# Kernel tuning notes

Hardware: AMD Instinct MI355X
Metric: run time of the kernel (lower is better)

Reference implementation:

```python
import jax, jax.numpy as jnp
import numpy as np

# Dims: B batch, T snippets, DV visual feat (1024), DA audio feat (128),
# H hid_dim (128), DF ffn dim (512), KC classifier kernel (7)
B, T, DV, DA, H, DF, KC = 128, 256, 1024, 128, 128, 512, 7


def _xavier(key, shape, fan_in, fan_out):
    a = (6.0 / (fan_in + fan_out)) ** 0.5
    return jax.random.uniform(key, shape, jnp.float32, -a, a)


def setup_inputs() -> dict:
    key = jax.random.key(0)
    ks = jax.random.split(key, 9)
    return {
        "x": jax.random.normal(ks[0], (B, T, DV + DA), jnp.float32),
        # CrossAttention: q from audio (DA->H), k,v from visual (DV->H), out proj H->DV
        "Wq": _xavier(ks[1], (DA, H), DA, H), "bq": jnp.zeros((H,), jnp.float32),
        "Wk": _xavier(ks[2], (DV, H), DV, H), "bk": jnp.zeros((H,), jnp.float32),
        "Wv": _xavier(ks[3], (DV, H), DV, H), "bv": jnp.zeros((H,), jnp.float32),
        "Wo": _xavier(ks[4], (H, DV), H, DV), "bo": jnp.zeros((DV,), jnp.float32),
        # LayerNorm over modal_a=1024
        "ln_g": jnp.ones((DV,), jnp.float32), "ln_b": jnp.zeros((DV,), jnp.float32),
        # FFN: Conv1d(1024,512,1) -> GELU -> Conv1d(512,128,1) == two linears over channels
        "W1": _xavier(ks[5], (DV, DF), DV, DF), "b1": jnp.zeros((DF,), jnp.float32),
        "W2": _xavier(ks[6], (DF, H), DF, H), "b2": jnp.zeros((H,), jnp.float32),
        # Classifier: Conv1d(128, 1, kernel=7), OIH layout
        "Wc": _xavier(ks[7], (1, H, KC), H * KC, KC), "bc": jnp.zeros((1,), jnp.float32),
    }


def _distance_adj(t: int) -> jnp.ndarray:
    # adj[i, j] = exp(-|i - j| / e)  (DistanceAdj from the repo)
    idx = jnp.arange(t, dtype=jnp.float32)
    return jnp.exp(-jnp.abs(idx[:, None] - idx[None, :]) / jnp.float32(np.e))


def reference(x, Wq, bq, Wk, bk, Wv, bv, Wo, bo, ln_g, ln_b, W1, b1, W2, b2, Wc, bc):
    f_v = x[:, :, :DV]   # [B, T, 1024]
    f_a = x[:, :, DV:]   # [B, T, 128]
    adj = _distance_adj(T)  # [T, T], broadcast over batch

    # Cross attention: query from audio, key/value from visual, adjacency bias
    q = f_a @ Wq + bq                               # [B, T, H]
    k = f_v @ Wk + bk                               # [B, T, H]
    v = f_v @ Wv + bv                               # [B, T, H]
    scores = jnp.einsum('bqh,bkh->bqk', q, k) / jnp.sqrt(jnp.float32(H)) + adj
    attn = jax.nn.softmax(scores, axis=-1)
    ctx = jnp.einsum('bqk,bkh->bqh', attn, v)       # [B, T, H]
    ca_out = ctx @ Wo + bo                          # [B, T, 1024]

    # residual + LayerNorm(modal_a)
    h = f_v + ca_out
    mu = jnp.mean(h, axis=-1, keepdims=True)
    var = jnp.mean(jnp.square(h - mu), axis=-1, keepdims=True)
    h = (h - mu) * jax.lax.rsqrt(var + 1e-5) * ln_g + ln_b

    # conv1d(k=1) FFN: 1024 -> 512 -> GELU -> 128 (dropout = identity at eval)
    h = jax.nn.gelu(h @ W1 + b1, approximate=False) @ W2 + b2   # [B, T, 128]

    # causal left pad 6, then Conv1d(128 -> 1, kernel 7)
    hc = jnp.pad(jnp.transpose(h, (0, 2, 1)), ((0, 0), (0, 0), (KC - 1, 0)))  # [B, 128, T+6]
    logits = jax.lax.conv_general_dilated(
        hc, Wc, window_strides=(1,), padding='VALID',
        dimension_numbers=('NCH', 'OIH', 'NCH')) + bc[None, :, None]           # [B, 1, T]
    return jax.nn.sigmoid(logits[:, 0, :])                                      # [B, T]
```

## Files before the change

kernel.cpp:

```cpp
#include <hip/hip_runtime.h>
#include <hip/hip_bf16.h>
#include <math.h>

#define BB 128
#define TT 256
#define DV 1024
#define DA 128
#define HH 128
#define DF 512
#define KC 7
#define MM (BB*TT)

typedef __attribute__((ext_vector_type(8))) short    short8v;
typedef __attribute__((ext_vector_type(8))) _Float16 half8v;
typedef __attribute__((ext_vector_type(4))) float    float4v;

__device__ __forceinline__ float gelu_exact(float v) {
    return 0.5f * v * (1.0f + erff(v * 0.70710678118654752f));
}
__device__ __forceinline__ ushort f2h(float f) {
    _Float16 h = (_Float16)f;
    return __builtin_bit_cast(ushort, h);
}
__device__ __forceinline__ float h2f(ushort u) {
    _Float16 h = __builtin_bit_cast(_Float16, u);
    return (float)h;
}

__global__ __launch_bounds__(256) void wconv_kernel(const float* __restrict__ W,
                                                    ushort* __restrict__ Th,
                                                    int K, int N)
{
    __shared__ float sT[64][65];
    const int n0 = blockIdx.x * 64, k0 = blockIdx.y * 64;
    const int t = threadIdx.x;
    const int kk = t >> 4, n4 = (t & 15) * 4;
#pragma unroll
    for (int i = 0; i < 4; ++i) {
        float4 f = *(const float4*)(W + (size_t)(k0 + kk + i * 16) * N + n0 + n4);
        sT[kk + i * 16][n4 + 0] = f.x;
        sT[kk + i * 16][n4 + 1] = f.y;
        sT[kk + i * 16][n4 + 2] = f.z;
        sT[kk + i * 16][n4 + 3] = f.w;
    }
    __syncthreads();
    const int n = t >> 2, kq = (t & 3) * 16;
    ushort hh[16];
#pragma unroll
    for (int j = 0; j < 16; ++j) hh[j] = f2h(sT[kq + j][n]);
    ushort* dh = Th + (size_t)(n0 + n) * K + k0 + kq;
#pragma unroll
    for (int j = 0; j < 16; j += 4)
        *(ushort4*)(dh + j) = make_ushort4(hh[j], hh[j+1], hh[j+2], hh[j+3]);
}

template<int BM, int A_F32, int OUT>
__global__ __launch_bounds__(256) void mgemm(const void* __restrict__ Av, int lda,
                                             const ushort* __restrict__ Bt,
                                             const float* __restrict__ bias,
                                             void* __restrict__ Cv,
                                             int N, int K)
{
    constexpr int MF = BM / 32;
    __shared__ ushort Ah[4][BM][8];
    __shared__ ushort Bh[4][128][8];

    const int tid = threadIdx.x;
    const int l = tid & 63;
    const int w = tid >> 6;
    const int wrow = (w >> 1) * (MF * 16), wcol = (w & 1) * 64;
    const int m0 = blockIdx.y * BM, n0 = blockIdx.x * 128;

    float4v acc[MF][4];
#pragma unroll
    for (int m = 0; m < MF; ++m)
#pragma unroll
        for (int n = 0; n < 4; ++n) acc[m][n] = (float4v){0.f, 0.f, 0.f, 0.f};

    for (int k0 = 0; k0 < K; k0 += 32) {
        __syncthreads();
        if (A_F32) {
            if (BM == 128) {
                const int srow = tid >> 1, kh = (tid & 1) * 16;
                const float* Ap = (const float*)Av + (size_t)(m0 + srow) * lda + k0 + kh;
#pragma unroll
                for (int i = 0; i < 4; ++i) {
                    float4 f = *(const float4*)(Ap + i * 4);
                    *(ushort4*)&Ah[(kh >> 3) + (i >> 1)][srow][(i & 1) * 4] =
                        make_ushort4(f2h(f.x), f2h(f.y), f2h(f.z), f2h(f.w));
                }
            } else {
                const int srow = tid >> 2, ko = (tid & 3) * 8;
                const float* Ap = (const float*)Av + (size_t)(m0 + srow) * lda + k0 + ko;
#pragma unroll
                for (int i = 0; i < 2; ++i) {
                    float4 f = *(const float4*)(Ap + i * 4);
                    *(ushort4*)&Ah[ko >> 3][srow][i * 4] =
                        make_ushort4(f2h(f.x), f2h(f.y), f2h(f.z), f2h(f.w));
                }
            }
        } else {
            if (BM == 128) {
                const int srow = tid >> 1, kh = (tid & 1) * 16;
                const ushort* Ap = (const ushort*)Av + (size_t)(m0 + srow) * lda + k0 + kh;
                *(short8v*)&Ah[(kh >> 3) + 0][srow][0] = *(const short8v*)(Ap + 0);
                *(short8v*)&Ah[(kh >> 3) + 1][srow][0] = *(const short8v*)(Ap + 8);
            } else {
                const int srow = tid >> 2, ko = (tid & 3) * 8;
                const ushort* Ap = (const ushort*)Av + (size_t)(m0 + srow) * lda + k0 + ko;
                *(short8v*)&Ah[ko >> 3][srow][0] = *(const short8v*)Ap;
            }
        }
        {
            const int srow = tid >> 1, kh = (tid & 1) * 16;
            const ushort* Bp = Bt + (size_t)(n0 + srow) * K + k0 + kh;
            *(short8v*)&Bh[(kh >> 3) + 0][srow][0] = *(const short8v*)(Bp + 0);
            *(short8v*)&Bh[(kh >> 3) + 1][srow][0] = *(const short8v*)(Bp + 8);
        }
        __syncthreads();

        const int g = l >> 4, lr = l & 15;
        half8v af[MF], bf_[4];
#pragma unroll
        for (int m = 0; m < MF; ++m)
            af[m] = *(const half8v*)&Ah[g][wrow + m * 16 + lr][0];
#pragma unroll
        for (int n = 0; n < 4; ++n)
            bf_[n] = *(const half8v*)&Bh[g][wcol + n * 16 + lr][0];
#pragma unroll
        for (int m = 0; m < MF; ++m)
#pragma unroll
            for (int n = 0; n < 4; ++n)
                acc[m][n] = __builtin_amdgcn_mfma_f32_16x16x32_f16(af[m], bf_[n], acc[m][n], 0, 0, 0);
    }

    const int g = l >> 4, lr = l & 15;
#pragma unroll
    for (int n = 0; n < 4; ++n) {
        const int col = n0 + wcol + n * 16 + lr;
        const float bv = bias[col];
#pragma unroll
        for (int m = 0; m < MF; ++m) {
#pragma unroll
            for (int r = 0; r < 4; ++r) {
                const int row = m0 + wrow + m * 16 + g * 4 + r;
                float o = acc[m][n][r] + bv;
                if (OUT == 0)      ((float*)Cv)[(size_t)row * N + col] = o;
                else if (OUT == 1) ((ushort*)Cv)[(size_t)row * N + col] = f2h(gelu_exact(o));
                else               ((ushort*)Cv)[(size_t)row * N + col] = f2h(o);
            }
        }
    }
}

__global__ __launch_bounds__(256) void scores_kernel(const float* __restrict__ q,
                                                     const float* __restrict__ k,
                                                     float* __restrict__ S)
{
    const int kh = blockIdx.x;
    const int qh = blockIdx.y;
    const int b  = blockIdx.z;
    const int tid = threadIdx.x;
    const int tr = tid >> 4;
    const int tc = tid & 15;

    __shared__ float sA[32][68];
    __shared__ float sB[32][132];

    const float* Ab = q + ((size_t)b * TT + qh * 64) * HH;
    const float* Bb = k + ((size_t)b * TT + kh * 128) * HH;

    float acc[4][8];
#pragma unroll
    for (int i = 0; i < 4; ++i)
#pragma unroll
        for (int j = 0; j < 8; ++j) acc[i][j] = 0.0f;

    for (int k0 = 0; k0 < 128; k0 += 32) {
        __syncthreads();
#pragma unroll
        for (int ll = 0; ll < 2; ++ll) {
            int f = tid + ll * 256;
            int row = f >> 3, c4 = f & 7;
            float4 val = *(const float4*)(Ab + (size_t)row * HH + k0 + c4 * 4);
            sA[c4 * 4 + 0][row] = val.x;
            sA[c4 * 4 + 1][row] = val.y;
            sA[c4 * 4 + 2][row] = val.z;
            sA[c4 * 4 + 3][row] = val.w;
        }
#pragma unroll
        for (int ll = 0; ll < 4; ++ll) {
            int f = tid + ll * 256;
            int row = f >> 3, c4 = f & 7;
            float4 val = *(const float4*)(Bb + (size_t)row * HH + k0 + c4 * 4);
            sB[c4 * 4 + 0][row] = val.x;
            sB[c4 * 4 + 1][row] = val.y;
            sB[c4 * 4 + 2][row] = val.z;
            sB[c4 * 4 + 3][row] = val.w;
        }
        __syncthreads();
#pragma unroll
        for (int kk = 0; kk < 32; ++kk) {
            float4 a4 = *(const float4*)&sA[kk][tr * 4];
            float4 b0 = *(const float4*)&sB[kk][tc * 8];
            float4 b1 = *(const float4*)&sB[kk][tc * 8 + 4];
            float a[4]  = {a4.x, a4.y, a4.z, a4.w};
            float bb[8] = {b0.x, b0.y, b0.z, b0.w, b1.x, b1.y, b1.z, b1.w};
#pragma unroll
            for (int i = 0; i < 4; ++i)
#pragma unroll
                for (int j = 0; j < 8; ++j) acc[i][j] += a[i] * bb[j];
        }
    }

    const float scale = 0.088388347648318447f;
    const float inv_e = 0.36787944117144233f;
#pragma unroll
    for (int i = 0; i < 4; ++i) {
        int rq = qh * 64 + tr * 4 + i;
        float* srow = S + ((size_t)b * TT + rq) * TT + kh * 128 + tc * 8;
        float o[8];
#pragma unroll
        for (int j = 0; j < 8; ++j) {
            int ck = kh * 128 + tc * 8 + j;
            float adj = expf(-fabsf((float)(rq - ck)) * inv_e);
            o[j] = acc[i][j] * scale + adj;
        }
        *(float4*)srow       = make_float4(o[0], o[1], o[2], o[3]);
        *(float4*)(srow + 4) = make_float4(o[4], o[5], o[6], o[7]);
    }
}

__global__ __launch_bounds__(256) void softmax_kernel(float* __restrict__ S)
{
    const int row  = blockIdx.x * 4 + (threadIdx.x >> 6);
    const int lane = threadIdx.x & 63;
    float* p = S + (size_t)row * TT + lane * 4;
    float4 v = *(float4*)p;
    float m = fmaxf(fmaxf(v.x, v.y), fmaxf(v.z, v.w));
#pragma unroll
    for (int mask = 1; mask < 64; mask <<= 1) m = fmaxf(m, __shfl_xor(m, mask));
    float e0 = expf(v.x - m), e1 = expf(v.y - m), e2 = expf(v.z - m), e3 = expf(v.w - m);
    float s = e0 + e1 + e2 + e3;
#pragma unroll
    for (int mask = 1; mask < 64; mask <<= 1) s += __shfl_xor(s, mask);
    float inv = 1.0f / s;
    *(float4*)p = make_float4(e0 * inv, e1 * inv, e2 * inv, e3 * inv);
}

__global__ __launch_bounds__(256) void pv_kernel(const float* __restrict__ S,
                                                 const float* __restrict__ v,
                                                 ushort* __restrict__ ctx)
{
    const int qh = blockIdx.x;
    const int b  = blockIdx.y;
    const int tid = threadIdx.x;
    const int tr = tid >> 4;
    const int tc = tid & 15;

    __shared__ float sA[32][68];
    __shared__ float sB[32][132];

    const float* Ab = S + ((size_t)b * TT + qh * 64) * TT;
    const float* Bb = v + (size_t)b * TT * HH;

    float acc[4][8];
#pragma unroll
    for (int i = 0; i < 4; ++i)
#pragma unroll
        for (int j = 0; j < 8; ++j) acc[i][j] = 0.0f;

    for (int k0 = 0; k0 < 256; k0 += 32) {
        __syncthreads();
#pragma unroll
        for (int ll = 0; ll < 2; ++ll) {
            int f = tid + ll * 256;
            int row = f >> 3, c4 = f & 7;
            float4 val = *(const float4*)(Ab + (size_t)row * TT + k0 + c4 * 4);
            sA[c4 * 4 + 0][row] = val.x;
            sA[c4 * 4 + 1][row] = val.y;
            sA[c4 * 4 + 2][row] = val.z;
            sA[c4 * 4 + 3][row] = val.w;
        }
#pragma unroll
        for (int ll = 0; ll < 4; ++ll) {
            int f = tid + ll * 256;
            int row = f >> 5, c4 = f & 31;
            float4 val = *(const float4*)(Bb + (size_t)(k0 + row) * HH + c4 * 4);
            *(float4*)&sB[row][c4 * 4] = val;
        }
        __syncthreads();
#pragma unroll
        for (int kk = 0; kk < 32; ++kk) {
            float4 a4 = *(const float4*)&sA[kk][tr * 4];
            float4 b0 = *(const float4*)&sB[kk][tc * 8];
            float4 b1 = *(const float4*)&sB[kk][tc * 8 + 4];
            float a[4]  = {a4.x, a4.y, a4.z, a4.w};
            float bb[8] = {b0.x, b0.y, b0.z, b0.w, b1.x, b1.y, b1.z, b1.w};
#pragma unroll
            for (int i = 0; i < 4; ++i)
#pragma unroll
                for (int j = 0; j < 8; ++j) acc[i][j] += a[i] * bb[j];
        }
    }

#pragma unroll
    for (int i = 0; i < 4; ++i) {
        ushort* crow = ctx + ((size_t)b * TT + qh * 64 + tr * 4 + i) * HH + tc * 8;
        *(ushort4*)crow       = make_ushort4(f2h(acc[i][0]), f2h(acc[i][1]),
                                             f2h(acc[i][2]), f2h(acc[i][3]));
        *(ushort4*)(crow + 4) = make_ushort4(f2h(acc[i][4]), f2h(acc[i][5]),
                                             f2h(acc[i][6]), f2h(acc[i][7]));
    }
}

__global__ __launch_bounds__(256) void resln_kernel(const float* __restrict__ x,
                                                    const ushort* __restrict__ ca16,
                                                    ushort* __restrict__ h16,
                                                    const float* __restrict__ gam,
                                                    const float* __restrict__ bet)
{
    const int row = blockIdx.x;
    const int tid = threadIdx.x;
    const float4 f = *(const float4*)(x + (size_t)row * 1152 + tid * 4);
    const ushort4 c4v = *(const ushort4*)(ca16 + (size_t)row * 1024 + tid * 4);
    float4 h;
    h.x = f.x + h2f(c4v.x); h.y = f.y + h2f(c4v.y);
    h.z = f.z + h2f(c4v.z); h.w = f.w + h2f(c4v.w);

    float s  = h.x + h.y + h.z + h.w;
    float ss = h.x * h.x + h.y * h.y + h.z * h.z + h.w * h.w;
#pragma unroll
    for (int m = 1; m < 64; m <<= 1) {
        s  += __shfl_xor(s, m);
        ss += __shfl_xor(ss, m);
    }
    __shared__ float red[8];
    if ((tid & 63) == 0) {
        red[tid >> 6]       = s;
        red[4 + (tid >> 6)] = ss;
    }
    __syncthreads();
    s  = red[0] + red[1] + red[2] + red[3];
    ss = red[4] + red[5] + red[6] + red[7];
    const float mean = s * (1.0f / 1024.0f);
    const float var  = ss * (1.0f / 1024.0f) - mean * mean;
    const float rstd = 1.0f / sqrtf(var + 1e-5f);

    const float4 g4 = *(const float4*)(gam + tid * 4);
    const float4 b4 = *(const float4*)(bet + tid * 4);
    ushort* hout = h16 + (size_t)row * 1024 + tid * 4;
    *(ushort4*)hout = make_ushort4(
        f2h((h.x - mean) * rstd * g4.x + b4.x),
        f2h((h.y - mean) * rstd * g4.y + b4.y),
        f2h((h.z - mean) * rstd * g4.z + b4.z),
        f2h((h.w - mean) * rstd * g4.w + b4.w));
}

__global__ __launch_bounds__(256) void conv_kernel(const float* __restrict__ h2,
                                                   const float* __restrict__ Wc,
                                                   const float* __restrict__ bcp,
                                                   float* __restrict__ out)
{
    const int t0 = blockIdx.x * 64;
    const int b  = blockIdx.y;
    const int tid = threadIdx.x;

    __shared__ float sw[896];
    __shared__ float sh[70][130];
    __shared__ float red[4][64];

    for (int i = tid; i < 896; i += 256) sw[i] = Wc[i];
    for (int f = tid; f < 70 * 32; f += 256) {
        int rr = f >> 5, c4 = f & 31;
        int trow = t0 - 6 + rr;
        float4 val = make_float4(0.f, 0.f, 0.f, 0.f);
        if (trow >= 0)
            val = *(const float4*)(h2 + ((size_t)b * TT + trow) * HH + c4 * 4);
        sh[rr][c4 * 4 + 0] = val.x;
        sh[rr][c4 * 4 + 1] = val.y;
        sh[rr][c4 * 4 + 2] = val.z;
        sh[rr][c4 * 4 + 3] = val.w;
    }
    __syncthreads();

    const int tt  = tid & 63;
    const int grp = tid >> 6;
    const int i0  = grp * 32;
    float acc = 0.0f;
    for (int j = 0; j < 7; ++j) {
        const int srow2 = tt + j;
#pragma unroll
        for (int i2 = 0; i2 < 16; ++i2) {
            float2 hv = *(const float2*)&sh[srow2][i0 + i2 * 2];
            acc += hv.x * sw[(i0 + i2 * 2) * 7 + j] + hv.y * sw[(i0 + i2 * 2 + 1) * 7 + j];
        }
    }
    red[grp][tt] = acc;
    __syncthreads();
    if (grp == 0) {
        float tot = red[0][tt] + red[1][tt] + red[2][tt] + red[3][tt] + bcp[0];
        out[(size_t)b * TT + t0 + tt] = 1.0f / (1.0f + expf(-tot));
    }
}

extern "C" void kernel_launch(void* const* d_in, const int* in_sizes, int n_in,
                              void* d_out, int out_size, void* d_ws, size_t ws_size,
                              hipStream_t stream)
{
    const float* x   = (const float*)d_in[0];
    const float* Wq  = (const float*)d_in[1];
    const float* bq  = (const float*)d_in[2];
    const float* Wk  = (const float*)d_in[3];
    const float* bk  = (const float*)d_in[4];
    const float* Wv  = (const float*)d_in[5];
    const float* bv  = (const float*)d_in[6];
    const float* Wo  = (const float*)d_in[7];
    const float* bo  = (const float*)d_in[8];
    const float* lng = (const float*)d_in[9];
    const float* lnb = (const float*)d_in[10];
    const float* W1  = (const float*)d_in[11];
    const float* b1  = (const float*)d_in[12];
    const float* W2  = (const float*)d_in[13];
    const float* b2  = (const float*)d_in[14];
    const float* Wc  = (const float*)d_in[15];
    const float* bc  = (const float*)d_in[16];
    float* out = (float*)d_out;
    char* wsb = (char*)d_ws;

    ushort* WT   = (ushort*)wsb;
    const size_t oWq = 0,      oWk = 16384,  oWv = 147456;
    const size_t oWo = 278528, oW1 = 409600, oW2 = 933888;
    float*  qb   = (float*)(wsb + 4194304);
    float*  kb   = qb + 4194304;
    float*  vb   = kb + 4194304;
    ushort* ctxb = (ushort*)(wsb + 54525952);
    float*  Sbuf = (float*)(wsb + 62914560);
    ushort* ca16 = (ushort*)(wsb + 62914560);
    ushort* h16  = (ushort*)(wsb + 130023424);
    ushort* hf   = (ushort*)(wsb + 4194304);
    float*  h2   = (float*)(wsb + 37748736);

    dim3 thr(256);
    wconv_kernel<<<dim3(2, 2),  thr, 0, stream>>>(Wq, WT + oWq, 128, 128);
    wconv_kernel<<<dim3(2, 16), thr, 0, stream>>>(Wk, WT + oWk, 1024, 128);
    wconv_kernel<<<dim3(2, 16), thr, 0, stream>>>(Wv, WT + oWv, 1024, 128);
    wconv_kernel<<<dim3(16, 2), thr, 0, stream>>>(Wo, WT + oWo, 128, 1024);
    wconv_kernel<<<dim3(8, 16), thr, 0, stream>>>(W1, WT + oW1, 1024, 512);
    wconv_kernel<<<dim3(2, 8),  thr, 0, stream>>>(W2, WT + oW2, 512, 128);

    mgemm<64, 1, 0><<<dim3(1, 512), thr, 0, stream>>>(x,        1152, WT + oWk, bk, kb, 128, 1024);
    mgemm<64, 1, 0><<<dim3(1, 512), thr, 0, stream>>>(x,        1152, WT + oWv, bv, vb, 128, 1024);
    mgemm<64, 1, 0><<<dim3(1, 512), thr, 0, stream>>>(x + 1024, 1152, WT + oWq, bq, qb, 128, 128);
    scores_kernel <<<dim3(2, 4, 128), thr, 0, stream>>>(qb, kb, Sbuf);
    softmax_kernel<<<dim3(MM / 4),    thr, 0, stream>>>(Sbuf);
    pv_kernel     <<<dim3(4, 128),    thr, 0, stream>>>(Sbuf, vb, ctxb);
    mgemm<128, 0, 2><<<dim3(8, 256), thr, 0, stream>>>(ctxb, 128, WT + oWo, bo, ca16, 1024, 128);
    resln_kernel<<<dim3(MM), thr, 0, stream>>>(x, ca16, h16, lng, lnb);
    mgemm<128, 0, 1><<<dim3(4, 256), thr, 0, stream>>>(h16, 1024, WT + oW1, b1, hf, 512, 1024);
    mgemm<64, 0, 0><<<dim3(1, 512), thr, 0, stream>>>(hf, 512, WT + oW2, b2, h2, 128, 512);
    conv_kernel<<<dim3(4, 128), thr, 0, stream>>>(h2, Wc, bc, out);
}
```

Before: 568.8 us.

## Fuse K/V projections into one GEMM, stage epilogue via LDS, swizzle blocks

Concatenates the transposed Wk and Wv weights and their biases so one GEMM with N=256 produces an interleaved KV buffer, reading the visual activations once instead of twice. The scores and PV kernels now read K and V from that buffer with a 256 stride. The mgemm epilogue stages output tiles in shared memory and writes them back as vectorized rows instead of scattered scalar stores. It also remaps block indices so that neighbouring blocks are spread across XCDs. These add extra syncs and a tiny concat kernel.

```diff
diff --git a/kernel.cpp b/kernel.cpp
--- a/kernel.cpp
+++ b/kernel.cpp
@@ -54,6 +54,14 @@
         *(ushort4*)(dh + j) = make_ushort4(hh[j], hh[j+1], hh[j+2], hh[j+3]);
 }
 
+__global__ __launch_bounds__(256) void bcat_kernel(const float* __restrict__ a,
+                                                   const float* __restrict__ b,
+                                                   float* __restrict__ dst)
+{
+    const int t = threadIdx.x;
+    dst[t] = (t < 128) ? a[t] : b[t - 128];
+}
+
 template<int BM, int A_F32, int OUT>
 __global__ __launch_bounds__(256) void mgemm(const void* __restrict__ Av, int lda,
                                              const ushort* __restrict__ Bt,
@@ -62,14 +70,20 @@
                                              int N, int K)
 {
     constexpr int MF = BM / 32;
-    __shared__ ushort Ah[4][BM][8];
-    __shared__ ushort Bh[4][128][8];
+    __shared__ __align__(16) ushort smem[8192];
+    auto Ah = (ushort (*)[BM][8])(smem);
+    auto Bh = (ushort (*)[128][8])(smem + 4 * BM * 8);
+
+    const int nwg = gridDim.x * gridDim.y;
+    const int hid = blockIdx.y * gridDim.x + blockIdx.x;
+    const int d   = (hid & 7) * (nwg >> 3) + (hid >> 3);
+    const int bx  = d % gridDim.x, by = d / gridDim.x;
 
     const int tid = threadIdx.x;
     const int l = tid & 63;
     const int w = tid >> 6;
     const int wrow = (w >> 1) * (MF * 16), wcol = (w & 1) * 64;
-    const int m0 = blockIdx.y * BM, n0 = blockIdx.x * 128;
+    const int m0 = by * BM, n0 = bx * 128;
 
     float4v acc[MF][4];
 #pragma unroll
@@ -134,27 +148,55 @@
                 acc[m][n] = __builtin_amdgcn_mfma_f32_16x16x32_f16(af[m], bf_[n], acc[m][n], 0, 0, 0);
     }
 
-    const int g = l >> 4, lr = l & 15;
-#pragma unroll
-    for (int n = 0; n < 4; ++n) {
-        const int col = n0 + wcol + n * 16 + lr;
-        const float bv = bias[col];
-#pragma unroll
-        for (int m = 0; m < MF; ++m) {
-#pragma unroll
-            for (int r = 0; r < 4; ++r) {
-                const int row = m0 + wrow + m * 16 + g * 4 + r;
-                float o = acc[m][n][r] + bv;
-                if (OUT == 0)      ((float*)Cv)[(size_t)row * N + col] = o;
-                else if (OUT == 1) ((ushort*)Cv)[(size_t)row * N + col] = f2h(gelu_exact(o));
-                else               ((ushort*)Cv)[(size_t)row * N + col] = f2h(o);
+    {
+        const int g2 = l >> 4, lr = l & 15;
+        constexpr int RPP = (OUT == 0) ? 32 : 64;
+#pragma unroll
+        for (int row0 = 0; row0 < BM; row0 += RPP) {
+            __syncthreads();
+#pragma unroll
+            for (int m = 0; m < MF; ++m) {
+                const int rbase = wrow + m * 16 + g2 * 4;
+                if (rbase >= row0 && rbase < row0 + RPP) {
+#pragma unroll
+                    for (int n = 0; n < 4; ++n) {
+                        const int col = wcol + n * 16 + lr;
+                        const float bv = bias[n0 + col];
+#pragma unroll
+                        for (int r = 0; r < 4; ++r) {
+                            const float o = acc[m][n][r] + bv;
+                            const int lrow = rbase + r - row0;
+                            if (OUT == 0)      ((float*)smem)[lrow * 128 + col] = o;
+                            else if (OUT == 1) smem[lrow * 128 + col] = f2h(gelu_exact(o));
+                            else               smem[lrow * 128 + col] = f2h(o);
+                        }
+                    }
+                }
             }
+            __syncthreads();
+            if (OUT == 0) {
+#pragma unroll
+                for (int it = 0; it < (RPP * 128) / (4 * 256); ++it) {
+                    const int u = tid + it * 256;
+                    const int rr = u >> 5, cc = (u & 31) * 4;
+                    *(float4*)&((float*)Cv)[(size_t)(m0 + row0 + rr) * N + n0 + cc] =
+                        *(float4*)&((float*)smem)[rr * 128 + cc];
+                }
+            } else {
+#pragma unroll
+                for (int it = 0; it < (RPP * 128) / (8 * 256); ++it) {
+                    const int u = tid + it * 256;
+                    const int rr = u >> 4, cc = (u & 15) * 8;
+                    *(short8v*)&((ushort*)Cv)[(size_t)(m0 + row0 + rr) * N + n0 + cc] =
+                        *(short8v*)&smem[rr * 128 + cc];
+                }
+            }
         }
     }
 }
 
 __global__ __launch_bounds__(256) void scores_kernel(const float* __restrict__ q,
-                                                     const float* __restrict__ k,
+                                                     const float* __restrict__ kv,
                                                      float* __restrict__ S)
 {
     const int kh = blockIdx.x;
@@ -168,7 +210,7 @@
     __shared__ float sB[32][132];
 
     const float* Ab = q + ((size_t)b * TT + qh * 64) * HH;
-    const float* Bb = k + ((size_t)b * TT + kh * 128) * HH;
+    const float* Bb = kv + ((size_t)b * TT + kh * 128) * 256;
 
     float acc[4][8];
 #pragma unroll
@@ -192,7 +234,7 @@
         for (int ll = 0; ll < 4; ++ll) {
             int f = tid + ll * 256;
             int row = f >> 3, c4 = f & 7;
-            float4 val = *(const float4*)(Bb + (size_t)row * HH + k0 + c4 * 4);
+            float4 val = *(const float4*)(Bb + (size_t)row * 256 + k0 + c4 * 4);
             sB[c4 * 4 + 0][row] = val.x;
             sB[c4 * 4 + 1][row] = val.y;
             sB[c4 * 4 + 2][row] = val.z;
@@ -249,7 +291,7 @@
 }
 
 __global__ __launch_bounds__(256) void pv_kernel(const float* __restrict__ S,
-                                                 const float* __restrict__ v,
+                                                 const float* __restrict__ kv,
                                                  ushort* __restrict__ ctx)
 {
     const int qh = blockIdx.x;
@@ -262,7 +304,7 @@
     __shared__ float sB[32][132];
 
     const float* Ab = S + ((size_t)b * TT + qh * 64) * TT;
-    const float* Bb = v + (size_t)b * TT * HH;
+    const float* Bb = kv + (size_t)b * TT * 256 + 128;
 
     float acc[4][8];
 #pragma unroll
@@ -286,7 +328,7 @@
         for (int ll = 0; ll < 4; ++ll) {
             int f = tid + ll * 256;
             int row = f >> 5, c4 = f & 31;
-            float4 val = *(const float4*)(Bb + (size_t)(k0 + row) * HH + c4 * 4);
+            float4 val = *(const float4*)(Bb + (size_t)(k0 + row) * 256 + c4 * 4);
             *(float4*)&sB[row][c4 * 4] = val;
         }
         __syncthreads();
@@ -429,11 +471,14 @@
     char* wsb = (char*)d_ws;
 
     ushort* WT   = (ushort*)wsb;
-    const size_t oWq = 0,      oWk = 16384,  oWv = 147456;
-    const size_t oWo = 278528, oW1 = 409600, oW2 = 933888;
+    const size_t oWq  = 0;
+    const size_t oWkv = 16384;
+    const size_t oWo  = 278528;
+    const size_t oW1  = 409600;
+    const size_t oW2  = 933888;
+    float*  bkv  = (float*)(wsb + 2097152);
     float*  qb   = (float*)(wsb + 4194304);
-    float*  kb   = qb + 4194304;
-    float*  vb   = kb + 4194304;
+    float*  kvb  = (float*)(wsb + 20971520);
     ushort* ctxb = (ushort*)(wsb + 54525952);
     float*  Sbuf = (float*)(wsb + 62914560);
     ushort* ca16 = (ushort*)(wsb + 62914560);
@@ -443,18 +488,18 @@
 
     dim3 thr(256);
     wconv_kernel<<<dim3(2, 2),  thr, 0, stream>>>(Wq, WT + oWq, 128, 128);
-    wconv_kernel<<<dim3(2, 16), thr, 0, stream>>>(Wk, WT + oWk, 1024, 128);
-    wconv_kernel<<<dim3(2, 16), thr, 0, stream>>>(Wv, WT + oWv, 1024, 128);
+    wconv_kernel<<<dim3(2, 16), thr, 0, stream>>>(Wk, WT + oWkv, 1024, 128);
+    wconv_kernel<<<dim3(2, 16), thr, 0, stream>>>(Wv, WT + oWkv + 128 * 1024, 1024, 128);
     wconv_kernel<<<dim3(16, 2), thr, 0, stream>>>(Wo, WT + oWo, 128, 1024);
     wconv_kernel<<<dim3(8, 16), thr, 0, stream>>>(W1, WT + oW1, 1024, 512);
     wconv_kernel<<<dim3(2, 8),  thr, 0, stream>>>(W2, WT + oW2, 512, 128);
-
-    mgemm<64, 1, 0><<<dim3(1, 512), thr, 0, stream>>>(x,        1152, WT + oWk, bk, kb, 128, 1024);
-    mgemm<64, 1, 0><<<dim3(1, 512), thr, 0, stream>>>(x,        1152, WT + oWv, bv, vb, 128, 1024);
-    mgemm<64, 1, 0><<<dim3(1, 512), thr, 0, stream>>>(x + 1024, 1152, WT + oWq, bq, qb, 128, 128);
-    scores_kernel <<<dim3(2, 4, 128), thr, 0, stream>>>(qb, kb, Sbuf);
+    bcat_kernel<<<dim3(1), thr, 0, stream>>>(bk, bv, bkv);
+
+    mgemm<64, 1, 0><<<dim3(2, 512), thr, 0, stream>>>(x,        1152, WT + oWkv, bkv, kvb, 256, 1024);
+    mgemm<64, 1, 0><<<dim3(1, 512), thr, 0, stream>>>(x + 1024, 1152, WT + oWq,  bq,  qb,  128, 128);
+    scores_kernel <<<dim3(2, 4, 128), thr, 0, stream>>>(qb, kvb, Sbuf);
     softmax_kernel<<<dim3(MM / 4),    thr, 0, stream>>>(Sbuf);
-    pv_kernel     <<<dim3(4, 128),    thr, 0, stream>>>(Sbuf, vb, ctxb);
+    pv_kernel     <<<dim3(4, 128),    thr, 0, stream>>>(Sbuf, kvb, ctxb);
     mgemm<128, 0, 2><<<dim3(8, 256), thr, 0, stream>>>(ctxb, 128, WT + oWo, bo, ca16, 1024, 128);
     resln_kernel<<<dim3(MM), thr, 0, stream>>>(x, ca16, h16, lng, lnb);
     mgemm<128, 0, 1><<<dim3(4, 256), thr, 0, stream>>>(h16, 1024, WT + oW1, b1, hf, 512, 1024);
```

New measurement: 588.0 us. 3.4% more time.
